# Kernel tuning notes

Measured on AMD Instinct MI355X. Metric: run time of the kernel, lower is better.

## Reference

```python
import jax, jax.numpy as jnp
import numpy as np

DIM = 1024
HEADS = 16
DIM_HEAD = 64
INNER = HEADS * DIM_HEAD  # 1024
SCALE = DIM_HEAD ** -0.5


def setup_inputs() -> dict:
    key = jax.random.key(0)
    k_x, k_qkv, k_ow, k_ob = jax.random.split(key, 4)
    B, N = 4, 2048
    x = jax.random.normal(k_x, (B, N, DIM), dtype=jnp.float32)
    # nn.Linear weights stored as [out, in] in torch; keep [in, out] for x @ W.
    w_qkv = jax.random.normal(k_qkv, (DIM, 3 * INNER), dtype=jnp.float32) * (DIM ** -0.5)
    w_out = jax.random.normal(k_ow, (INNER, DIM), dtype=jnp.float32) * (INNER ** -0.5)
    b_out = jax.random.normal(k_ob, (DIM,), dtype=jnp.float32) * 0.01
    return {"x": x, "w_qkv": w_qkv, "w_out": w_out, "b_out": b_out}


def reference(x, w_qkv, w_out, b_out):
    B, N, _ = x.shape
    qkv = x @ w_qkv  # [B, N, 3*inner]
    q, k, v = jnp.split(qkv, 3, axis=-1)
    # [B, N, inner] -> [B, H, N, dh]
    def to_heads(t):
        return t.reshape(B, N, HEADS, DIM_HEAD).transpose(0, 2, 1, 3)
    q, k, v = to_heads(q), to_heads(k), to_heads(v)
    attn = jnp.einsum("bhqd,bhkd->bhqk", q, k) * SCALE  # [B, H, N, N]
    attn = jax.nn.softmax(attn, axis=-1)
    out = jnp.einsum("bhqk,bhkd->bhqd", attn, v)  # [B, H, N, dh]
    out = out.transpose(0, 2, 1, 3).reshape(B, N, INNER)
    return out @ w_out + b_out
```

## Files before the change

kernel.cpp:

```cpp
#include <hip/hip_runtime.h>
#include <hip/hip_bf16.h>
#include <stdint.h>

typedef __attribute__((ext_vector_type(4))) float f32x4;
typedef __attribute__((ext_vector_type(16))) float f32x16;
typedef __attribute__((ext_vector_type(8))) short s16x8;
typedef __attribute__((ext_vector_type(4))) short s16x4;
typedef __attribute__((ext_vector_type(4))) unsigned int u32x4;

#define DEV static __device__ __forceinline__

constexpr int B_ = 4, H_ = 16, N_ = 2048;
constexpr float CL_ = 0.18033688011112042f;

DEV short f2bf(float x) {
  __hip_bfloat16 h = __float2bfloat16(x);
  return *reinterpret_cast<short*>(&h);
}

DEV uint32_t cvtpk(float lo, float hi) {
  uint32_t r;
  asm("v_cvt_pk_bf16_f32 %0, %1, %2" : "=v"(r) : "v"(lo), "v"(hi));
  return r;
}

DEV void gload16(const void* g, void* l) {
  __builtin_amdgcn_global_load_lds((const __attribute__((address_space(1))) void*)g,
                                   (__attribute__((address_space(3))) void*)l, 16, 0, 0);
}

__global__ void k_cvt(const float* __restrict__ x, short* __restrict__ xb) {
  int i = (blockIdx.x * 256 + threadIdx.x) * 8;
  const float4* p = reinterpret_cast<const float4*>(x + i);
  float4 a = p[0], b = p[1];
  s16x8 o;
  o[0] = f2bf(a.x); o[1] = f2bf(a.y); o[2] = f2bf(a.z); o[3] = f2bf(a.w);
  o[4] = f2bf(b.x); o[5] = f2bf(b.y); o[6] = f2bf(b.z); o[7] = f2bf(b.w);
  *reinterpret_cast<s16x8*>(xb + i) = o;
}

__global__ void k_tw(const float* __restrict__ W, short* __restrict__ WT, int R, int C) {
  __shared__ short t[64][72];
  int r0 = blockIdx.y * 64, c0 = blockIdx.x * 64;
  int tid = threadIdx.x;
  int r = tid >> 2, cp = (tid & 3) * 16;
  const float4* s4 = reinterpret_cast<const float4*>(W + (size_t)(r0 + r) * C + c0 + cp);
  float4 f0 = s4[0], f1 = s4[1], f2 = s4[2], f3 = s4[3];
  short* tr = &t[r][cp];
  tr[0] = f2bf(f0.x); tr[1] = f2bf(f0.y); tr[2]  = f2bf(f0.z); tr[3]  = f2bf(f0.w);
  tr[4] = f2bf(f1.x); tr[5] = f2bf(f1.y); tr[6]  = f2bf(f1.z); tr[7]  = f2bf(f1.w);
  tr[8] = f2bf(f2.x); tr[9] = f2bf(f2.y); tr[10] = f2bf(f2.z); tr[11] = f2bf(f2.w);
  tr[12] = f2bf(f3.x); tr[13] = f2bf(f3.y); tr[14] = f2bf(f3.z); tr[15] = f2bf(f3.w);
  __syncthreads();
  int cc = tid >> 2, rp = (tid & 3) * 16;
  short buf[16];
#pragma unroll
  for (int i = 0; i < 16; ++i) buf[i] = t[rp + i][cc];
  short* dst = WT + (size_t)(c0 + cc) * R + r0 + rp;
  *reinterpret_cast<s16x8*>(dst) = *reinterpret_cast<s16x8*>(buf);
  *reinterpret_cast<s16x8*>(dst + 8) = *reinterpret_cast<s16x8*>(buf + 8);
}

__global__ void k_tv(const short* __restrict__ v, short* __restrict__ vT) {
  __shared__ short t[64][72];
  int bh = blockIdx.y, n0 = blockIdx.x * 64;
  int tid = threadIdx.x;
  int r = tid >> 2, cp = (tid & 3) * 16;
  const short* src = v + ((size_t)bh * N_ + n0 + r) * 64 + cp;
  *reinterpret_cast<s16x8*>(&t[r][cp]) = *reinterpret_cast<const s16x8*>(src);
  *reinterpret_cast<s16x8*>(&t[r][cp + 8]) = *reinterpret_cast<const s16x8*>(src + 8);
  __syncthreads();
  int d = tid >> 2, np = (tid & 3) * 16;
  short buf[16];
#pragma unroll
  for (int i = 0; i < 16; ++i) buf[i] = t[np + i][d];
  short* dst = vT + ((size_t)bh * 64 + d) * N_ + n0 + np;
  *reinterpret_cast<s16x8*>(dst) = *reinterpret_cast<s16x8*>(buf);
  *reinterpret_cast<s16x8*>(dst + 8) = *reinterpret_cast<s16x8*>(buf + 8);
}

template <int EPI>
__global__ __launch_bounds__(256, 2)
void k_gemm(const short* __restrict__ A, const short* __restrict__ BT,
            int M, int N, int K,
            short* __restrict__ oq, short* __restrict__ ok, short* __restrict__ ov,
            const float* __restrict__ bias, float* __restrict__ out) {
  __shared__ short As[128 * 32];
  __shared__ short Bs[128 * 32];
  const int tid = threadIdx.x;
  const int m0 = blockIdx.x * 128, n0 = blockIdx.y * 128;
  const int lane = tid & 63, w = tid >> 6, g = lane >> 4, c = lane & 15;
  const int wr = w >> 1, wc = w & 1;
  f32x4 acc[4][4] = {};
  const int trow = tid >> 2, tk = (tid & 3) * 8;
  const short* ga = A + (size_t)(m0 + trow) * K + tk;
  const short* gb = BT + (size_t)(n0 + trow) * K + tk;
  short* la = As + tid * 8;
  short* lb = Bs + tid * 8;
  for (int k0 = 0; k0 < K; k0 += 32) {
    gload16(ga + k0, la);
    gload16(ga + (size_t)64 * K + k0, la + 2048);
    gload16(gb + k0, lb);
    gload16(gb + (size_t)64 * K + k0, lb + 2048);
    __syncthreads();
    s16x8 af[4], bf[4];
#pragma unroll
    for (int i = 0; i < 4; ++i)
      af[i] = *reinterpret_cast<const s16x8*>(As + (wr * 64 + i * 16 + c) * 32 + g * 8);
#pragma unroll
    for (int j = 0; j < 4; ++j)
      bf[j] = *reinterpret_cast<const s16x8*>(Bs + (wc * 64 + j * 16 + c) * 32 + g * 8);
#pragma unroll
    for (int i = 0; i < 4; ++i)
#pragma unroll
      for (int j = 0; j < 4; ++j)
        acc[i][j] = __builtin_amdgcn_mfma_f32_16x16x32_bf16(af[i], bf[j], acc[i][j], 0, 0, 0);
    __syncthreads();
  }
  if (EPI == 0) {
#pragma unroll
    for (int bj = 0; bj < 4; ++bj) {
      int ncol = n0 + wc * 64 + bj * 16 + c;
      int part = ncol >> 10;
      int c10 = ncol & 1023;
      int h = c10 >> 6, d = c10 & 63;
      short* dst0 = part == 0 ? oq : (part == 1 ? ok : ov);
      float qs = (part == 0) ? CL_ : 1.0f;
#pragma unroll
      for (int ai = 0; ai < 4; ++ai) {
#pragma unroll
        for (int r = 0; r < 4; ++r) {
          int mrow = m0 + wr * 64 + ai * 16 + g * 4 + r;
          int b = mrow >> 11, nr = mrow & 2047;
          dst0[((size_t)((b * H_ + h) * N_ + nr) << 6) + d] = f2bf(acc[ai][bj][r] * qs);
        }
      }
    }
  } else {
#pragma unroll
    for (int bj = 0; bj < 4; ++bj) {
      int ncol = n0 + wc * 64 + bj * 16 + c;
      float bb = bias[ncol];
#pragma unroll
      for (int ai = 0; ai < 4; ++ai) {
#pragma unroll
        for (int r = 0; r < 4; ++r) {
          int mrow = m0 + wr * 64 + ai * 16 + g * 4 + r;
          out[(size_t)mrow * N + ncol] = acc[ai][bj][r] + bb;
        }
      }
    }
  }
}

__global__ __launch_bounds__(256, 2)
void k_attn(const short* __restrict__ q, const short* __restrict__ kk,
            const short* __restrict__ vT, short* __restrict__ ao) {
  __shared__ __align__(16) char smem[32768];
  int bh = blockIdx.x, qb = blockIdx.y;
  int b = bh >> 4, head = bh & 15;
  int tid = threadIdx.x, w = tid >> 6, lane = tid & 63;
  int half = lane >> 5, qc = lane & 31;
  const size_t ho = (size_t)bh * (N_ * 64);
  const char* Kc = reinterpret_cast<const char*>(kk + ho);
  const char* Vc = reinterpret_cast<const char*>(vT + ho);
  const short* Q = q + ho;
  int q0w = qb * 256 + w * 64;
  s16x8 qf[2][4];
#pragma unroll
  for (int i = 0; i < 2; ++i)
#pragma unroll
    for (int ks = 0; ks < 4; ++ks)
      qf[i][ks] = *reinterpret_cast<const s16x8*>(Q + (size_t)(q0w + i * 32 + qc) * 64 + ks * 16 + half * 8);
  f32x16 ot[2][2] = {};
  float lp[2] = {0.f, 0.f};
  const int rsw = (qc & 7) << 4;
  const int s_i0 = tid, s_i1 = tid + 256;
  const int s_r0 = s_i0 >> 3, s_c0 = ((s_i0 & 7) << 4) ^ ((s_r0 & 7) << 4);
  const int s_r1 = s_i1 >> 3, s_c1 = ((s_i1 & 7) << 4) ^ ((s_r1 & 7) << 4);
  {
    char* kb_ = smem;
    gload16(Kc + (size_t)s_r0 * 128 + s_c0, kb_ + s_i0 * 16);
    gload16(Kc + (size_t)s_r1 * 128 + s_c1, kb_ + s_i1 * 16);
    gload16(Vc + (size_t)s_r0 * 4096 + s_c0, kb_ + 8192 + s_i0 * 16);
    gload16(Vc + (size_t)s_r1 * 4096 + s_c1, kb_ + 8192 + s_i1 * 16);
  }
  __syncthreads();
  int cur = 0;
  for (int tt = 0; tt < N_ / 64; ++tt) {
    if (tt + 1 < N_ / 64) {
      char* nb = smem + (cur ^ 1) * 16384;
      gload16(Kc + (size_t)((tt + 1) * 64 + s_r0) * 128 + s_c0, nb + s_i0 * 16);
      gload16(Kc + (size_t)((tt + 1) * 64 + s_r1) * 128 + s_c1, nb + s_i1 * 16);
      gload16(Vc + (size_t)s_r0 * 4096 + (tt + 1) * 128 + s_c0, nb + 8192 + s_i0 * 16);
      gload16(Vc + (size_t)s_r1 * 4096 + (tt + 1) * 128 + s_c1, nb + 8192 + s_i1 * 16);
    }
    const char* kb_ = smem + cur * 16384;
    const char* vb_ = kb_ + 8192;
    s16x8 kf[2][4];
#pragma unroll
    for (int j = 0; j < 2; ++j)
#pragma unroll
      for (int ks = 0; ks < 4; ++ks)
        kf[j][ks] = *reinterpret_cast<const s16x8*>(kb_ + (j * 32 + qc) * 128 + ((ks * 32 + half * 16) ^ rsw));
    f32x16 st[2][2] = {};
    __builtin_amdgcn_s_setprio(1);
#pragma unroll
    for (int j = 0; j < 2; ++j)
#pragma unroll
      for (int i = 0; i < 2; ++i)
#pragma unroll
        for (int ks = 0; ks < 4; ++ks)
          st[j][i] = __builtin_amdgcn_mfma_f32_32x32x16_bf16(kf[j][ks], qf[i][ks], st[j][i], 0, 0, 0);
    __builtin_amdgcn_s_setprio(0);
#pragma unroll
    for (int j = 0; j < 2; ++j)
#pragma unroll
      for (int i = 0; i < 2; ++i)
#pragma unroll
        for (int r = 0; r < 16; ++r) {
          float p = __builtin_amdgcn_exp2f(st[j][i][r]);
          st[j][i][r] = p;
          lp[i] += p;
        }
    u32x4 pwv[2][4];
#pragma unroll
    for (int j = 0; j < 2; ++j)
#pragma unroll
      for (int i = 0; i < 2; ++i)
#pragma unroll
        for (int bb = 0; bb < 2; ++bb)
#pragma unroll
          for (int p = 0; p < 2; ++p) {
            uint32_t Aw = cvtpk(st[j][i][8 * bb + 2 * p], st[j][i][8 * bb + 2 * p + 1]);
            uint32_t Bw = cvtpk(st[j][i][8 * bb + 4 + 2 * p], st[j][i][8 * bb + 4 + 2 * p + 1]);
            asm volatile("v_permlane32_swap_b32 %0, %1" : "+v"(Aw), "+v"(Bw));
            pwv[i][j * 2 + bb][p] = Aw;
            pwv[i][j * 2 + bb][p + 2] = Bw;
          }
    s16x8 vf[2][4];
#pragma unroll
    for (int db = 0; db < 2; ++db)
#pragma unroll
      for (int kb4 = 0; kb4 < 4; ++kb4)
        vf[db][kb4] = *reinterpret_cast<const s16x8*>(vb_ + (db * 32 + qc) * 128 + ((kb4 * 32 + half * 16) ^ rsw));
    __builtin_amdgcn_s_setprio(1);
#pragma unroll
    for (int db = 0; db < 2; ++db)
#pragma unroll
      for (int i = 0; i < 2; ++i)
#pragma unroll
        for (int kb4 = 0; kb4 < 4; ++kb4)
          ot[db][i] = __builtin_amdgcn_mfma_f32_32x32x16_bf16(
              vf[db][kb4], __builtin_bit_cast(s16x8, pwv[i][kb4]), ot[db][i], 0, 0, 0);
    __builtin_amdgcn_s_setprio(0);
    __syncthreads();
    cur ^= 1;
  }
  float inv[2];
#pragma unroll
  for (int i = 0; i < 2; ++i) {
    float t = lp[i] + __shfl_xor(lp[i], 32, 64);
    inv[i] = 1.f / t;
  }
  __syncthreads();
  short* Oq = reinterpret_cast<short*>(smem) + w * 2304;
#pragma unroll
  for (int i = 0; i < 2; ++i) {
#pragma unroll
    for (int db = 0; db < 2; ++db)
#pragma unroll
      for (int m = 0; m < 4; ++m) {
        uint2 pk;
        pk.x = cvtpk(ot[db][i][4 * m] * inv[i], ot[db][i][4 * m + 1] * inv[i]);
        pk.y = cvtpk(ot[db][i][4 * m + 2] * inv[i], ot[db][i][4 * m + 3] * inv[i]);
        *reinterpret_cast<uint2*>(Oq + qc * 72 + db * 32 + m * 8 + half * 4) = pk;
      }
    int q2 = lane >> 1, dcol = (lane & 1) * 32;
    size_t ro = (size_t)(b * N_ + q0w + i * 32 + q2) * 1024 + head * 64 + dcol;
#pragma unroll
    for (int ch = 0; ch < 4; ++ch) {
      s16x8 vv = *reinterpret_cast<const s16x8*>(Oq + q2 * 72 + dcol + ch * 8);
      *reinterpret_cast<s16x8*>(ao + ro + ch * 8) = vv;
    }
  }
}

extern "C" void kernel_launch(void* const* d_in, const int* in_sizes, int n_in,
                              void* d_out, int out_size, void* d_ws, size_t ws_size,
                              hipStream_t stream) {
  const float* x = (const float*)d_in[0];
  const float* w_qkv = (const float*)d_in[1];
  const float* w_out = (const float*)d_in[2];
  const float* b_out = (const float*)d_in[3];
  float* out = (float*)d_out;
  char* ws = (char*)d_ws;
  short* xb    = (short*)(ws);
  short* wqkvT = (short*)(ws + 16777216);
  short* woutT = (short*)(ws + 23068672);
  short* qB    = (short*)(ws + 25165824);
  short* kB    = (short*)(ws + 41943040);
  short* vtmp  = (short*)(ws + 58720256);
  short* vTT   = (short*)(ws + 75497472);
  short* ao    = xb;

  k_cvt<<<4096, 256, 0, stream>>>(x, xb);
  k_tw<<<dim3(48, 16), 256, 0, stream>>>(w_qkv, wqkvT, 1024, 3072);
  k_tw<<<dim3(16, 16), 256, 0, stream>>>(w_out, woutT, 1024, 1024);
  k_gemm<0><<<dim3(64, 24), 256, 0, stream>>>(xb, wqkvT, 8192, 3072, 1024,
                                              qB, kB, vtmp, nullptr, nullptr);
  k_tv<<<dim3(32, 64), 256, 0, stream>>>(vtmp, vTT);
  k_attn<<<dim3(64, 8), 256, 0, stream>>>(qB, kB, vTT, ao);
  k_gemm<1><<<dim3(64, 8), 256, 0, stream>>>(ao, woutT, 8192, 1024, 1024,
                                             nullptr, nullptr, nullptr, b_out, out);
}
```

Baseline: 193.8 us.

## Load K/V fragments directly from global into registers, dropping LDS staging

The attention kernel no longer stages K and V tiles through double-buffered shared memory with async loads and block barriers. Each wave now reads its K and V MFMA fragments straight from global memory into registers, prefetching the next K tile during the PV MFMAs and removing the per-iteration __syncthreads. The intent is to cut LDS traffic and barrier stalls. The cost is that all four waves redundantly fetch the same K/V data through the cache hierarchy, and the V loads sit right before their use, so memory latency may be exposed.

```diff
diff --git a/kernel.cpp b/kernel.cpp
--- a/kernel.cpp
+++ b/kernel.cpp
@@ -156,15 +156,15 @@
 __global__ __launch_bounds__(256, 2)
 void k_attn(const short* __restrict__ q, const short* __restrict__ kk,
             const short* __restrict__ vT, short* __restrict__ ao) {
-  __shared__ __align__(16) char smem[32768];
+  __shared__ __align__(16) short Oq_all[4][2304];
   int bh = blockIdx.x, qb = blockIdx.y;
   int b = bh >> 4, head = bh & 15;
   int tid = threadIdx.x, w = tid >> 6, lane = tid & 63;
   int half = lane >> 5, qc = lane & 31;
   const size_t ho = (size_t)bh * (N_ * 64);
+  const short* Q = q + ho;
   const char* Kc = reinterpret_cast<const char*>(kk + ho);
   const char* Vc = reinterpret_cast<const char*>(vT + ho);
-  const short* Q = q + ho;
   int q0w = qb * 256 + w * 64;
   s16x8 qf[2][4];
 #pragma unroll
@@ -174,35 +174,14 @@
       qf[i][ks] = *reinterpret_cast<const s16x8*>(Q + (size_t)(q0w + i * 32 + qc) * 64 + ks * 16 + half * 8);
   f32x16 ot[2][2] = {};
   float lp[2] = {0.f, 0.f};
-  const int rsw = (qc & 7) << 4;
-  const int s_i0 = tid, s_i1 = tid + 256;
-  const int s_r0 = s_i0 >> 3, s_c0 = ((s_i0 & 7) << 4) ^ ((s_r0 & 7) << 4);
-  const int s_r1 = s_i1 >> 3, s_c1 = ((s_i1 & 7) << 4) ^ ((s_r1 & 7) << 4);
-  {
-    char* kb_ = smem;
-    gload16(Kc + (size_t)s_r0 * 128 + s_c0, kb_ + s_i0 * 16);
-    gload16(Kc + (size_t)s_r1 * 128 + s_c1, kb_ + s_i1 * 16);
-    gload16(Vc + (size_t)s_r0 * 4096 + s_c0, kb_ + 8192 + s_i0 * 16);
-    gload16(Vc + (size_t)s_r1 * 4096 + s_c1, kb_ + 8192 + s_i1 * 16);
-  }
-  __syncthreads();
-  int cur = 0;
+  s16x8 kf[2][4];
+#pragma unroll
+  for (int j = 0; j < 2; ++j)
+#pragma unroll
+    for (int ks = 0; ks < 4; ++ks)
+      kf[j][ks] = *reinterpret_cast<const s16x8*>(Kc + (size_t)(j * 32 + qc) * 128 + ks * 32 + half * 16);
   for (int tt = 0; tt < N_ / 64; ++tt) {
-    if (tt + 1 < N_ / 64) {
-      char* nb = smem + (cur ^ 1) * 16384;
-      gload16(Kc + (size_t)((tt + 1) * 64 + s_r0) * 128 + s_c0, nb + s_i0 * 16);
-      gload16(Kc + (size_t)((tt + 1) * 64 + s_r1) * 128 + s_c1, nb + s_i1 * 16);
-      gload16(Vc + (size_t)s_r0 * 4096 + (tt + 1) * 128 + s_c0, nb + 8192 + s_i0 * 16);
-      gload16(Vc + (size_t)s_r1 * 4096 + (tt + 1) * 128 + s_c1, nb + 8192 + s_i1 * 16);
-    }
-    const char* kb_ = smem + cur * 16384;
-    const char* vb_ = kb_ + 8192;
-    s16x8 kf[2][4];
-#pragma unroll
-    for (int j = 0; j < 2; ++j)
-#pragma unroll
-      for (int ks = 0; ks < 4; ++ks)
-        kf[j][ks] = *reinterpret_cast<const s16x8*>(kb_ + (j * 32 + qc) * 128 + ((ks * 32 + half * 16) ^ rsw));
+    int kv0 = tt * 64;
     f32x16 st[2][2] = {};
     __builtin_amdgcn_s_setprio(1);
 #pragma unroll
@@ -213,6 +192,12 @@
         for (int ks = 0; ks < 4; ++ks)
           st[j][i] = __builtin_amdgcn_mfma_f32_32x32x16_bf16(kf[j][ks], qf[i][ks], st[j][i], 0, 0, 0);
     __builtin_amdgcn_s_setprio(0);
+    s16x8 vf[2][4];
+#pragma unroll
+    for (int db = 0; db < 2; ++db)
+#pragma unroll
+      for (int kb4 = 0; kb4 < 4; ++kb4)
+        vf[db][kb4] = *reinterpret_cast<const s16x8*>(Vc + (size_t)(db * 32 + qc) * 4096 + kv0 * 2 + kb4 * 32 + half * 16);
 #pragma unroll
     for (int j = 0; j < 2; ++j)
 #pragma unroll
@@ -238,12 +223,13 @@
             pwv[i][j * 2 + bb][p] = Aw;
             pwv[i][j * 2 + bb][p + 2] = Bw;
           }
-    s16x8 vf[2][4];
-#pragma unroll
-    for (int db = 0; db < 2; ++db)
-#pragma unroll
-      for (int kb4 = 0; kb4 < 4; ++kb4)
-        vf[db][kb4] = *reinterpret_cast<const s16x8*>(vb_ + (db * 32 + qc) * 128 + ((kb4 * 32 + half * 16) ^ rsw));
+    if (tt + 1 < N_ / 64) {
+#pragma unroll
+      for (int j = 0; j < 2; ++j)
+#pragma unroll
+        for (int ks = 0; ks < 4; ++ks)
+          kf[j][ks] = *reinterpret_cast<const s16x8*>(Kc + (size_t)((tt + 1) * 64 + j * 32 + qc) * 128 + ks * 32 + half * 16);
+    }
     __builtin_amdgcn_s_setprio(1);
 #pragma unroll
     for (int db = 0; db < 2; ++db)
@@ -254,8 +240,6 @@
           ot[db][i] = __builtin_amdgcn_mfma_f32_32x32x16_bf16(
               vf[db][kb4], __builtin_bit_cast(s16x8, pwv[i][kb4]), ot[db][i], 0, 0, 0);
     __builtin_amdgcn_s_setprio(0);
-    __syncthreads();
-    cur ^= 1;
   }
   float inv[2];
 #pragma unroll
@@ -263,8 +247,7 @@
     float t = lp[i] + __shfl_xor(lp[i], 32, 64);
     inv[i] = 1.f / t;
   }
-  __syncthreads();
-  short* Oq = reinterpret_cast<short*>(smem) + w * 2304;
+  short* Oq = Oq_all[w];
 #pragma unroll
   for (int i = 0; i < 2; ++i) {
 #pragma unroll
```

After: 234.3 us. 20.9% more time.

## Use four-slot LDS ring with two-tile-ahead K/V prefetch in attention

Applied to the files above, without the earlier changes.

Replaces the double-buffered K/V staging in the attention kernel with a 4-slot, 64KB shared-memory ring. Each iteration issues loads two tiles ahead and waits with explicit vmcnt counts before a single barrier. The trailing per-iteration __syncthreads and the barrier before the epilogue are dropped, which relies on the ring spacing to keep reads and writes apart. The aim is to hide global-load latency better and cut barrier stalls, at the cost of doubling LDS per block, which could limit occupancy.

```diff
diff --git a/kernel.cpp b/kernel.cpp
--- a/kernel.cpp
+++ b/kernel.cpp
@@ -156,15 +156,16 @@
 __global__ __launch_bounds__(256, 2)
 void k_attn(const short* __restrict__ q, const short* __restrict__ kk,
             const short* __restrict__ vT, short* __restrict__ ao) {
-  __shared__ __align__(16) char smem[32768];
+  __shared__ __align__(16) char smem[65536];
+  constexpr int NT = N_ / 64;
   int bh = blockIdx.x, qb = blockIdx.y;
   int b = bh >> 4, head = bh & 15;
   int tid = threadIdx.x, w = tid >> 6, lane = tid & 63;
   int half = lane >> 5, qc = lane & 31;
   const size_t ho = (size_t)bh * (N_ * 64);
+  const short* Q = q + ho;
   const char* Kc = reinterpret_cast<const char*>(kk + ho);
   const char* Vc = reinterpret_cast<const char*>(vT + ho);
-  const short* Q = q + ho;
   int q0w = qb * 256 + w * 64;
   s16x8 qf[2][4];
 #pragma unroll
@@ -178,24 +179,28 @@
   const int s_i0 = tid, s_i1 = tid + 256;
   const int s_r0 = s_i0 >> 3, s_c0 = ((s_i0 & 7) << 4) ^ ((s_r0 & 7) << 4);
   const int s_r1 = s_i1 >> 3, s_c1 = ((s_i1 & 7) << 4) ^ ((s_r1 & 7) << 4);
-  {
-    char* kb_ = smem;
-    gload16(Kc + (size_t)s_r0 * 128 + s_c0, kb_ + s_i0 * 16);
-    gload16(Kc + (size_t)s_r1 * 128 + s_c1, kb_ + s_i1 * 16);
-    gload16(Vc + (size_t)s_r0 * 4096 + s_c0, kb_ + 8192 + s_i0 * 16);
-    gload16(Vc + (size_t)s_r1 * 4096 + s_c1, kb_ + 8192 + s_i1 * 16);
-  }
-  __syncthreads();
-  int cur = 0;
-  for (int tt = 0; tt < N_ / 64; ++tt) {
-    if (tt + 1 < N_ / 64) {
-      char* nb = smem + (cur ^ 1) * 16384;
-      gload16(Kc + (size_t)((tt + 1) * 64 + s_r0) * 128 + s_c0, nb + s_i0 * 16);
-      gload16(Kc + (size_t)((tt + 1) * 64 + s_r1) * 128 + s_c1, nb + s_i1 * 16);
-      gload16(Vc + (size_t)s_r0 * 4096 + (tt + 1) * 128 + s_c0, nb + 8192 + s_i0 * 16);
-      gload16(Vc + (size_t)s_r1 * 4096 + (tt + 1) * 128 + s_c1, nb + 8192 + s_i1 * 16);
+#define STAGE(T)                                                                       \
+  {                                                                                    \
+    char* nb = smem + ((T) & 3) * 16384;                                               \
+    gload16(Kc + (size_t)((T) * 64 + s_r0) * 128 + s_c0, nb + s_i0 * 16);              \
+    gload16(Kc + (size_t)((T) * 64 + s_r1) * 128 + s_c1, nb + s_i1 * 16);              \
+    gload16(Vc + (size_t)s_r0 * 4096 + (T) * 128 + s_c0, nb + 8192 + s_i0 * 16);       \
+    gload16(Vc + (size_t)s_r1 * 4096 + (T) * 128 + s_c1, nb + 8192 + s_i1 * 16);       \
+  }
+  STAGE(0);
+  STAGE(1);
+  for (int tt = 0; tt < NT; ++tt) {
+    if (tt + 2 < NT) STAGE(tt + 2);
+    if (tt + 2 < NT) {
+      asm volatile("s_waitcnt vmcnt(8)" ::: "memory");
+    } else if (tt + 1 < NT) {
+      asm volatile("s_waitcnt vmcnt(4)" ::: "memory");
+    } else {
+      asm volatile("s_waitcnt vmcnt(0)" ::: "memory");
     }
-    const char* kb_ = smem + cur * 16384;
+    __builtin_amdgcn_s_barrier();
+    __builtin_amdgcn_sched_barrier(0);
+    const char* kb_ = smem + (tt & 3) * 16384;
     const char* vb_ = kb_ + 8192;
     s16x8 kf[2][4];
 #pragma unroll
@@ -254,16 +259,14 @@
           ot[db][i] = __builtin_amdgcn_mfma_f32_32x32x16_bf16(
               vf[db][kb4], __builtin_bit_cast(s16x8, pwv[i][kb4]), ot[db][i], 0, 0, 0);
     __builtin_amdgcn_s_setprio(0);
-    __syncthreads();
-    cur ^= 1;
-  }
+  }
+#undef STAGE
   float inv[2];
 #pragma unroll
   for (int i = 0; i < 2; ++i) {
     float t = lp[i] + __shfl_xor(lp[i], 32, 64);
     inv[i] = 1.f / t;
   }
-  __syncthreads();
   short* Oq = reinterpret_cast<short*>(smem) + w * 2304;
 #pragma unroll
   for (int i = 0; i < 2; ++i) {
```

Result: no change. 191.8 us (-1.0%).
